# Optimization experiments

Hardware: AMD Instinct MI355X
Metric: run time of the kernel (lower is better)

The kernel has to match this reference:

```python
import jax, jax.numpy as jnp
import numpy as np

N, IN_DIM, OUT_DIM, H = 8192, 512, 512, 1
BN_EPS = 1e-5


def _lin(key, fan_in, fan_out):
    k1, k2 = jax.random.split(key)
    b = 1.0 / np.sqrt(fan_in)
    W = jax.random.uniform(k1, (fan_in, fan_out), jnp.float32, -b, b)
    bias = jax.random.uniform(k2, (fan_out,), jnp.float32, -b, b)
    return W, bias


def setup_inputs() -> dict:
    key = jax.random.key(0)
    ks = jax.random.split(key, 12)
    h = jax.random.normal(ks[0], (N, IN_DIM), jnp.float32)
    A = (jax.random.uniform(ks[1], (N, N)) < 0.01).astype(jnp.float32)
    qw, qb = _lin(ks[2], IN_DIM, OUT_DIM * H)
    kw, kb = _lin(ks[3], IN_DIM, OUT_DIM * H)
    vw, vb = _lin(ks[4], IN_DIM, OUT_DIM * H)
    ow, ob = _lin(ks[5], OUT_DIM, OUT_DIM)
    f1w, f1b = _lin(ks[6], OUT_DIM, OUT_DIM * 2)
    f2w, f2b = _lin(ks[7], OUT_DIM * 2, OUT_DIM)
    bn1_g = jax.random.normal(ks[8], (OUT_DIM,)) * 0.1 + 1.0
    bn1_b = jax.random.normal(ks[9], (OUT_DIM,)) * 0.1
    bn1_m = jax.random.normal(ks[10], (OUT_DIM,)) * 0.1
    bn1_v = jax.random.uniform(ks[11], (OUT_DIM,), jnp.float32, 0.5, 1.5)
    ks2 = jax.random.split(jax.random.fold_in(key, 7), 4)
    bn2_g = jax.random.normal(ks2[0], (OUT_DIM,)) * 0.1 + 1.0
    bn2_b = jax.random.normal(ks2[1], (OUT_DIM,)) * 0.1
    bn2_m = jax.random.normal(ks2[2], (OUT_DIM,)) * 0.1
    bn2_v = jax.random.uniform(ks2[3], (OUT_DIM,), jnp.float32, 0.5, 1.5)
    return dict(A=A, h=h, qw=qw, qb=qb, kw=kw, kb=kb, vw=vw, vb=vb,
                ow=ow, ob=ob, f1w=f1w, f1b=f1b, f2w=f2w, f2b=f2b,
                bn1_g=bn1_g, bn1_b=bn1_b, bn1_m=bn1_m, bn1_v=bn1_v,
                bn2_g=bn2_g, bn2_b=bn2_b, bn2_m=bn2_m, bn2_v=bn2_v)


def _bn_eval(x, g, b, m, v):
    return (x - m) * jax.lax.rsqrt(v + BN_EPS) * g + b


def reference(A, h, qw, qb, kw, kb, vw, vb, ow, ob, f1w, f1b, f2w, f2b,
              bn1_g, bn1_b, bn1_m, bn1_v, bn2_g, bn2_b, bn2_m, bn2_v):
    n = h.shape[0]
    scaling = OUT_DIM ** (-0.5)
    # q/k/v: [N, D, H] as in torch reshape of [N, D*H]
    q = (h @ qw + qb).reshape(n, OUT_DIM, H) * scaling
    k = (h @ kw + kb).reshape(n, OUT_DIM, H)
    v = (h @ vw + vb).reshape(n, OUT_DIM, H)
    qh = jnp.transpose(q, (2, 0, 1))          # (H, N, D)
    kh = jnp.transpose(k, (2, 1, 0))          # (H, D, N)
    vh = jnp.transpose(v, (2, 0, 1))          # (H, N, D)
    attn = jnp.einsum('hnd,hdm->hnm', qh, kh) * A[None]   # (H, N, N)
    attn = jax.nn.softmax(attn, axis=0)        # NOTE: softmax over HEAD axis, as in source
    out = jnp.einsum('hnm,hmd->hnd', attn, vh).reshape(n, H * OUT_DIM)
    # GTLayer (eval mode: dropout = identity, BN uses running stats)
    x = out @ ow + ob
    x = x + h                                  # residual
    x = _bn_eval(x, bn1_g, bn1_b, bn1_m, bn1_v)
    h2 = x
    f = jax.nn.relu(x @ f1w + f1b) @ f2w + f2b
    x = h2 + f
    x = _bn_eval(x, bn2_g, bn2_b, bn2_m, bn2_v)
    return x
```

## Files before the change

kernel.cpp:

```cpp
#include <hip/hip_runtime.h>

#define NROWS 8192
#define DIM 512
#define HID 1024
#define BN_EPS 1e-5f

typedef unsigned short ushort_t;
typedef __attribute__((ext_vector_type(8))) __bf16 bf16x8;
typedef __attribute__((ext_vector_type(4))) float f32x4;

union U4 {
    uint4 u;
    bf16x8 b;
    ushort_t s[8];
};

static __device__ __forceinline__ ushort_t f2b(float f) {
    union { float f; unsigned int i; } c;
    c.f = f;
    unsigned int i = c.i;
    unsigned int r = (i + 0x7FFFu + ((i >> 16) & 1u)) >> 16;
    return (ushort_t)r;
}

static __device__ __forceinline__ void gload_lds16(const ushort_t* g, ushort_t* l) {
    __builtin_amdgcn_global_load_lds((const __attribute__((address_space(1))) void*)g,
                                     (__attribute__((address_space(3))) void*)l, 16, 0, 0);
}

__global__ void colsum_kernel(const float* __restrict__ h, float* __restrict__ hs) {
    __shared__ float red[512];
    int t = threadIdx.x;
    int col0 = (t & 127) * 4;
    int rsub = t >> 7;
    int row0 = blockIdx.x * 32;
    float acc[4] = {0.f, 0.f, 0.f, 0.f};
#pragma unroll
    for (int r = 0; r < 16; ++r) {
        int row = row0 + r * 2 + rsub;
        float4 v = *(const float4*)(h + (size_t)row * DIM + col0);
        acc[0] += v.x; acc[1] += v.y; acc[2] += v.z; acc[3] += v.w;
    }
    if (rsub) {
#pragma unroll
        for (int j = 0; j < 4; ++j) red[col0 + j] = acc[j];
    }
    __syncthreads();
    if (!rsub) {
#pragma unroll
        for (int j = 0; j < 4; ++j) atomicAdd(&hs[col0 + j], acc[j] + red[col0 + j]);
    }
}

__global__ void matvec_kernel(const float* __restrict__ xin, const float* __restrict__ W,
                              const float* __restrict__ bvec, float scaleB,
                              float* __restrict__ outv) {
    __shared__ float red[8][32];
    int t = threadIdx.x;
    int col = blockIdx.x * 32 + (t & 31);
    int ks = t >> 5;
    float s = 0.f;
    for (int ki = 0; ki < 64; ++ki) {
        int k = ks * 64 + ki;
        s += xin[k] * W[k * 512 + col];
    }
    red[ks][t & 31] = s;
    __syncthreads();
    if (ks == 0) {
        float tot = scaleB * bvec[col];
#pragma unroll
        for (int r = 0; r < 8; ++r) tot += red[r][t & 31];
        outv[col] = tot;
    }
}

__global__ void matvec_prep_kernel(const float* __restrict__ xin, const float* __restrict__ W,
                                   const float* __restrict__ bvec,
                                   const float* g1, const float* b1,
                                   const float* m1, const float* v1,
                                   const float* g2, const float* b2,
                                   const float* m2, const float* v2,
                                   float* __restrict__ p, float* __restrict__ q0,
                                   float* __restrict__ a2v, float* __restrict__ c2v) {
    __shared__ float red[8][32];
    int t = threadIdx.x;
    int col = blockIdx.x * 32 + (t & 31);
    int ks = t >> 5;
    float s = 0.f;
    for (int ki = 0; ki < 64; ++ki) {
        int k = ks * 64 + ki;
        s += xin[k] * W[k * 512 + col];
    }
    red[ks][t & 31] = s;
    __syncthreads();
    if (ks == 0) {
        float tot = bvec[col];
#pragma unroll
        for (int r = 0; r < 8; ++r) tot += red[r][t & 31];
        float a1 = g1[col] * rsqrtf(v1[col] + BN_EPS);
        float c1 = b1[col] - m1[col] * a1;
        p[col] = a1;
        q0[col] = tot * a1 + c1;
        float a2 = g2[col] * rsqrtf(v2[col] + BN_EPS);
        a2v[col] = a2;
        c2v[col] = b2[col] - m2[col] * a2;
    }
}

__global__ void misc_kernel(const float* __restrict__ f1w, ushort_t* __restrict__ W1T,
                            const float* __restrict__ f2w, ushort_t* __restrict__ W2T,
                            const float* __restrict__ h, const float* __restrict__ p,
                            const float* __restrict__ q0, ushort_t* __restrict__ x1) {
    __shared__ float tile[32][33];
    int bid = blockIdx.x;
    if (bid >= 1024) {
        int idx = ((bid - 1024) * 256 + threadIdx.x) * 8;
        int d0 = idx & (DIM - 1);
        float4 h0 = *(const float4*)(h + idx);
        float4 h1 = *(const float4*)(h + idx + 4);
        U4 o;
        o.s[0] = f2b(h0.x * p[d0 + 0] + q0[d0 + 0]);
        o.s[1] = f2b(h0.y * p[d0 + 1] + q0[d0 + 1]);
        o.s[2] = f2b(h0.z * p[d0 + 2] + q0[d0 + 2]);
        o.s[3] = f2b(h0.w * p[d0 + 3] + q0[d0 + 3]);
        o.s[4] = f2b(h1.x * p[d0 + 4] + q0[d0 + 4]);
        o.s[5] = f2b(h1.y * p[d0 + 5] + q0[d0 + 5]);
        o.s[6] = f2b(h1.z * p[d0 + 6] + q0[d0 + 6]);
        o.s[7] = f2b(h1.w * p[d0 + 7] + q0[d0 + 7]);
        *(uint4*)(x1 + idx) = o.u;
        return;
    }
    const float* in;
    ushort_t* out;
    int R, C, bx, by;
    if (bid < 512) {
        in = f1w; out = W1T; R = 512; C = 1024;
        bx = (bid & 31) * 32; by = (bid >> 5) * 32;
    } else {
        int b = bid - 512;
        in = f2w; out = W2T; R = 1024; C = 512;
        bx = (b & 15) * 32; by = (b >> 4) * 32;
    }
    int tx = threadIdx.x & 31, ty = threadIdx.x >> 5;
#pragma unroll
    for (int i = 0; i < 32; i += 8)
        tile[ty + i][tx] = in[(by + ty + i) * C + bx + tx];
    __syncthreads();
#pragma unroll
    for (int i = 0; i < 32; i += 8)
        out[(bx + ty + i) * R + by + tx] = f2b(tile[tx][ty + i]);
}

template <int ROWS>
static __device__ __forceinline__ void stage_tile(const ushort_t* __restrict__ g, int ldg,
                                                  ushort_t* lds, int tid) {
#pragma unroll
    for (int it = 0; it < (ROWS * 8) / 256; ++it) {
        int c = it * 256 + tid;
        int row = c >> 3;
        int kc = (c & 7) << 3;
        const ushort_t* gp = g + (size_t)row * ldg + kc;
        ushort_t* lp = lds + ((it * 256 + (tid & 192)) << 3);
        gload_lds16(gp, lp);
    }
}

template <int NJ, bool RELU, bool FUSE>
__global__ __launch_bounds__(256) void gemm_kernel(
    const ushort_t* __restrict__ A, const ushort_t* __restrict__ BT,
    const float* __restrict__ bias, ushort_t* __restrict__ Cb,
    float* __restrict__ Cf, int M, int Nn, int K,
    const float* __restrict__ h, const float* __restrict__ p,
    const float* __restrict__ q0, const float* __restrict__ a2,
    const float* __restrict__ c2) {
    constexpr int BN = NJ * 32;
    constexpr int BK = 64;
    __shared__ ushort_t As[128 * BK];
    __shared__ ushort_t Bs[BN * BK];
    int tid = threadIdx.x;
    int lane = tid & 63, w = tid >> 6;
    int wm = (w & 1) * 64, wn = (w >> 1) * (NJ * 16);
    int bm = blockIdx.y * 128, bn = blockIdx.x * BN;

    f32x4 acc[4][NJ] = {};

    const ushort_t* Ag = A + (size_t)bm * K;
    const ushort_t* Bg = BT + (size_t)bn * K;

    for (int k0 = 0; k0 < K; k0 += BK) {
        __syncthreads();
        stage_tile<128>(Ag + k0, K, As, tid);
        stage_tile<BN>(Bg + k0, K, Bs, tid);
        __syncthreads();
#pragma unroll
        for (int ks = 0; ks < 2; ++ks) {
            int koff = ks * 32 + (lane >> 4) * 8;
            bf16x8 af[4], bfr[NJ];
#pragma unroll
            for (int i = 0; i < 4; ++i) {
                U4 t;
                t.u = *(const uint4*)(As + (wm + i * 16 + (lane & 15)) * BK + koff);
                af[i] = t.b;
            }
#pragma unroll
            for (int j = 0; j < NJ; ++j) {
                U4 t;
                t.u = *(const uint4*)(Bs + (wn + j * 16 + (lane & 15)) * BK + koff);
                bfr[j] = t.b;
            }
#pragma unroll
            for (int i = 0; i < 4; ++i)
#pragma unroll
                for (int j = 0; j < NJ; ++j)
                    acc[i][j] = __builtin_amdgcn_mfma_f32_16x16x32_bf16(af[i], bfr[j], acc[i][j], 0, 0, 0);
        }
    }

#pragma unroll
    for (int i = 0; i < 4; ++i) {
        int row0 = bm + wm + i * 16 + (lane >> 4) * 4;
#pragma unroll
        for (int j = 0; j < NJ; ++j) {
            int col = bn + wn + j * 16 + (lane & 15);
            float bv = bias[col];
            if constexpr (FUSE) {
                float pv = p[col], qv = q0[col], av = a2[col], cv = c2[col];
#pragma unroll
                for (int r = 0; r < 4; ++r) {
                    int row = row0 + r;
                    float hv = h[(size_t)row * DIM + col];
                    float x1v = hv * pv + qv;
                    Cf[(size_t)row * Nn + col] = (x1v + acc[i][j][r] + bv) * av + cv;
                }
            } else {
#pragma unroll
                for (int r = 0; r < 4; ++r) {
                    float v = acc[i][j][r] + bv;
                    if (RELU) v = fmaxf(v, 0.f);
                    Cb[(size_t)(row0 + r) * Nn + col] = f2b(v);
                }
            }
        }
    }
}

extern "C" void kernel_launch(void* const* d_in, const int* in_sizes, int n_in,
                              void* d_out, int out_size, void* d_ws, size_t ws_size,
                              hipStream_t stream) {
    const float* h = (const float*)d_in[1];
    const float* vw = (const float*)d_in[6];
    const float* vb = (const float*)d_in[7];
    const float* ow = (const float*)d_in[8];
    const float* ob = (const float*)d_in[9];
    const float* f1w = (const float*)d_in[10];
    const float* f1b = (const float*)d_in[11];
    const float* f2w = (const float*)d_in[12];
    const float* f2b = (const float*)d_in[13];
    const float* g1 = (const float*)d_in[14];
    const float* b1 = (const float*)d_in[15];
    const float* m1 = (const float*)d_in[16];
    const float* v1 = (const float*)d_in[17];
    const float* g2 = (const float*)d_in[18];
    const float* b2 = (const float*)d_in[19];
    const float* m2 = (const float*)d_in[20];
    const float* v2 = (const float*)d_in[21];
    float* out = (float*)d_out;

    char* ws = (char*)d_ws;
    float* hs = (float*)(ws + 0);
    float* pC = (float*)(ws + 2048);
    float* q0C = (float*)(ws + 4096);
    float* a2C = (float*)(ws + 6144);
    float* c2C = (float*)(ws + 8192);
    float* sBuf = (float*)(ws + 10240);
    ushort_t* X1 = (ushort_t*)(ws + 16384);
    ushort_t* Z = X1 + (size_t)NROWS * DIM;
    ushort_t* W1T = Z + (size_t)NROWS * HID;
    ushort_t* W2T = W1T + (size_t)HID * DIM;

    hipMemsetAsync(hs, 0, 512 * sizeof(float), stream);
    colsum_kernel<<<256, 256, 0, stream>>>(h, hs);
    matvec_kernel<<<16, 256, 0, stream>>>(hs, vw, vb, 8192.0f, sBuf);
    matvec_prep_kernel<<<16, 256, 0, stream>>>(sBuf, ow, ob, g1, b1, m1, v1,
                                               g2, b2, m2, v2, pC, q0C, a2C, c2C);
    misc_kernel<<<3072, 256, 0, stream>>>(f1w, W1T, f2w, W2T, h, pC, q0C, X1);
    gemm_kernel<4, true, false><<<dim3(8, 64), 256, 0, stream>>>(
        X1, W1T, f1b, Z, nullptr, NROWS, HID, DIM,
        nullptr, nullptr, nullptr, nullptr, nullptr);
    gemm_kernel<2, false, true><<<dim3(8, 64), 256, 0, stream>>>(
        Z, W2T, f2b, nullptr, out, NROWS, DIM, HID,
        h, pC, q0C, a2C, c2C);
}
```

Measured before the change: 428.9 us.

## Merge memset, column-sum and two matvec kernels into one cooperative kernel

```diff
diff --git a/kernel.cpp b/kernel.cpp
--- a/kernel.cpp
+++ b/kernel.cpp
@@ -1,4 +1,7 @@
 #include <hip/hip_runtime.h>
+#include <hip/hip_cooperative_groups.h>
+
+namespace cg = cooperative_groups;
 
 #define NROWS 8192
 #define DIM 512
@@ -28,82 +31,92 @@
                                      (__attribute__((address_space(3))) void*)l, 16, 0, 0);
 }
 
-__global__ void colsum_kernel(const float* __restrict__ h, float* __restrict__ hs) {
+__global__ __launch_bounds__(256) void prep_coop_kernel(
+    const float* __restrict__ h, float* __restrict__ hs,
+    const float* __restrict__ vw, const float* __restrict__ vb,
+    const float* __restrict__ ow, const float* __restrict__ ob,
+    const float* g1, const float* b1, const float* m1, const float* v1,
+    const float* g2, const float* b2, const float* m2, const float* v2,
+    float* __restrict__ sBuf,
+    float* __restrict__ p, float* __restrict__ q0,
+    float* __restrict__ a2v, float* __restrict__ c2v) {
+    cg::grid_group grid = cg::this_grid();
     __shared__ float red[512];
+    __shared__ float red2[8][32];
     int t = threadIdx.x;
-    int col0 = (t & 127) * 4;
-    int rsub = t >> 7;
-    int row0 = blockIdx.x * 32;
-    float acc[4] = {0.f, 0.f, 0.f, 0.f};
-#pragma unroll
-    for (int r = 0; r < 16; ++r) {
-        int row = row0 + r * 2 + rsub;
-        float4 v = *(const float4*)(h + (size_t)row * DIM + col0);
-        acc[0] += v.x; acc[1] += v.y; acc[2] += v.z; acc[3] += v.w;
-    }
-    if (rsub) {
-#pragma unroll
-        for (int j = 0; j < 4; ++j) red[col0 + j] = acc[j];
-    }
-    __syncthreads();
-    if (!rsub) {
-#pragma unroll
-        for (int j = 0; j < 4; ++j) atomicAdd(&hs[col0 + j], acc[j] + red[col0 + j]);
-    }
-}
-
-__global__ void matvec_kernel(const float* __restrict__ xin, const float* __restrict__ W,
-                              const float* __restrict__ bvec, float scaleB,
-                              float* __restrict__ outv) {
-    __shared__ float red[8][32];
-    int t = threadIdx.x;
-    int col = blockIdx.x * 32 + (t & 31);
-    int ks = t >> 5;
-    float s = 0.f;
-    for (int ki = 0; ki < 64; ++ki) {
-        int k = ks * 64 + ki;
-        s += xin[k] * W[k * 512 + col];
-    }
-    red[ks][t & 31] = s;
-    __syncthreads();
-    if (ks == 0) {
-        float tot = scaleB * bvec[col];
-#pragma unroll
-        for (int r = 0; r < 8; ++r) tot += red[r][t & 31];
-        outv[col] = tot;
-    }
-}
-
-__global__ void matvec_prep_kernel(const float* __restrict__ xin, const float* __restrict__ W,
-                                   const float* __restrict__ bvec,
-                                   const float* g1, const float* b1,
-                                   const float* m1, const float* v1,
-                                   const float* g2, const float* b2,
-                                   const float* m2, const float* v2,
-                                   float* __restrict__ p, float* __restrict__ q0,
-                                   float* __restrict__ a2v, float* __restrict__ c2v) {
-    __shared__ float red[8][32];
-    int t = threadIdx.x;
-    int col = blockIdx.x * 32 + (t & 31);
-    int ks = t >> 5;
-    float s = 0.f;
-    for (int ki = 0; ki < 64; ++ki) {
-        int k = ks * 64 + ki;
-        s += xin[k] * W[k * 512 + col];
-    }
-    red[ks][t & 31] = s;
-    __syncthreads();
-    if (ks == 0) {
-        float tot = bvec[col];
-#pragma unroll
-        for (int r = 0; r < 8; ++r) tot += red[r][t & 31];
-        float a1 = g1[col] * rsqrtf(v1[col] + BN_EPS);
-        float c1 = b1[col] - m1[col] * a1;
-        p[col] = a1;
-        q0[col] = tot * a1 + c1;
-        float a2 = g2[col] * rsqrtf(v2[col] + BN_EPS);
-        a2v[col] = a2;
-        c2v[col] = b2[col] - m2[col] * a2;
+    int b = blockIdx.x;
+
+    if (b == 0) {
+        hs[t] = 0.f;
+        hs[t + 256] = 0.f;
+    }
+    grid.sync();
+
+    {
+        int col0 = (t & 127) * 4;
+        int rsub = t >> 7;
+        int row0 = b * 32;
+        float acc[4] = {0.f, 0.f, 0.f, 0.f};
+#pragma unroll
+        for (int r = 0; r < 16; ++r) {
+            int row = row0 + r * 2 + rsub;
+            float4 v = *(const float4*)(h + (size_t)row * DIM + col0);
+            acc[0] += v.x; acc[1] += v.y; acc[2] += v.z; acc[3] += v.w;
+        }
+        if (rsub) {
+#pragma unroll
+            for (int j = 0; j < 4; ++j) red[col0 + j] = acc[j];
+        }
+        __syncthreads();
+        if (!rsub) {
+#pragma unroll
+            for (int j = 0; j < 4; ++j) atomicAdd(&hs[col0 + j], acc[j] + red[col0 + j]);
+        }
+    }
+    grid.sync();
+
+    if (b < 16) {
+        int col = b * 32 + (t & 31);
+        int ks = t >> 5;
+        float s = 0.f;
+        for (int ki = 0; ki < 64; ++ki) {
+            int k = ks * 64 + ki;
+            s += hs[k] * vw[k * 512 + col];
+        }
+        red2[ks][t & 31] = s;
+        __syncthreads();
+        if (ks == 0) {
+            float tot = 8192.0f * vb[col];
+#pragma unroll
+            for (int r = 0; r < 8; ++r) tot += red2[r][t & 31];
+            sBuf[col] = tot;
+        }
+        __syncthreads();
+    }
+    grid.sync();
+
+    if (b < 16) {
+        int col = b * 32 + (t & 31);
+        int ks = t >> 5;
+        float s = 0.f;
+        for (int ki = 0; ki < 64; ++ki) {
+            int k = ks * 64 + ki;
+            s += sBuf[k] * ow[k * 512 + col];
+        }
+        red2[ks][t & 31] = s;
+        __syncthreads();
+        if (ks == 0) {
+            float tot = ob[col];
+#pragma unroll
+            for (int r = 0; r < 8; ++r) tot += red2[r][t & 31];
+            float a1 = g1[col] * rsqrtf(v1[col] + BN_EPS);
+            float c1 = b1[col] - m1[col] * a1;
+            p[col] = a1;
+            q0[col] = tot * a1 + c1;
+            float a2 = g2[col] * rsqrtf(v2[col] + BN_EPS);
+            a2v[col] = a2;
+            c2v[col] = b2[col] - m2[col] * a2;
+        }
     }
 }
 
@@ -278,11 +291,13 @@
     ushort_t* W1T = Z + (size_t)NROWS * HID;
     ushort_t* W2T = W1T + (size_t)HID * DIM;
 
-    hipMemsetAsync(hs, 0, 512 * sizeof(float), stream);
-    colsum_kernel<<<256, 256, 0, stream>>>(h, hs);
-    matvec_kernel<<<16, 256, 0, stream>>>(hs, vw, vb, 8192.0f, sBuf);
-    matvec_prep_kernel<<<16, 256, 0, stream>>>(sBuf, ow, ob, g1, b1, m1, v1,
-                                               g2, b2, m2, v2, pC, q0C, a2C, c2C);
+    void* cargs[] = {(void*)&h, (void*)&hs, (void*)&vw, (void*)&vb,
+                     (void*)&ow, (void*)&ob,
+                     (void*)&g1, (void*)&b1, (void*)&m1, (void*)&v1,
+                     (void*)&g2, (void*)&b2, (void*)&m2, (void*)&v2,
+                     (void*)&sBuf, (void*)&pC, (void*)&q0C, (void*)&a2C, (void*)&c2C};
+    hipLaunchCooperativeKernel((void*)prep_coop_kernel, dim3(256), dim3(256),
+                               cargs, 0, stream);
     misc_kernel<<<3072, 256, 0, stream>>>(f1w, W1T, f2w, W2T, h, pC, q0C, X1);
     gemm_kernel<4, true, false><<<dim3(8, 64), 256, 0, stream>>>(
         X1, W1T, f1b, Z, nullptr, NROWS, HID, DIM,
```

Result: slower. 516.2 us (+20.4%).

## Fuse matvec chain with grid barrier and move weight transpose into colsum kernel

Applied to the files above, without the earlier changes.

```diff
diff --git a/kernel.cpp b/kernel.cpp
--- a/kernel.cpp
+++ b/kernel.cpp
@@ -28,127 +28,138 @@
                                      (__attribute__((address_space(3))) void*)l, 16, 0, 0);
 }
 
-__global__ void colsum_kernel(const float* __restrict__ h, float* __restrict__ hs) {
+__global__ void colsum_tr_kernel(const float* __restrict__ h, float* __restrict__ hs,
+                                 const float* __restrict__ f1w, ushort_t* __restrict__ W1T,
+                                 const float* __restrict__ f2w, ushort_t* __restrict__ W2T) {
     __shared__ float red[512];
+    __shared__ float tile[32][33];
+    int bid = blockIdx.x;
     int t = threadIdx.x;
-    int col0 = (t & 127) * 4;
-    int rsub = t >> 7;
-    int row0 = blockIdx.x * 32;
-    float acc[4] = {0.f, 0.f, 0.f, 0.f};
-#pragma unroll
-    for (int r = 0; r < 16; ++r) {
-        int row = row0 + r * 2 + rsub;
-        float4 v = *(const float4*)(h + (size_t)row * DIM + col0);
-        acc[0] += v.x; acc[1] += v.y; acc[2] += v.z; acc[3] += v.w;
-    }
-    if (rsub) {
-#pragma unroll
-        for (int j = 0; j < 4; ++j) red[col0 + j] = acc[j];
-    }
+    if (bid < 256) {
+        int col0 = (t & 127) * 4;
+        int rsub = t >> 7;
+        int row0 = bid * 32;
+        float acc[4] = {0.f, 0.f, 0.f, 0.f};
+#pragma unroll
+        for (int r = 0; r < 16; ++r) {
+            int row = row0 + r * 2 + rsub;
+            float4 v = *(const float4*)(h + (size_t)row * DIM + col0);
+            acc[0] += v.x; acc[1] += v.y; acc[2] += v.z; acc[3] += v.w;
+        }
+        if (rsub) {
+#pragma unroll
+            for (int j = 0; j < 4; ++j) red[col0 + j] = acc[j];
+        }
+        __syncthreads();
+        if (!rsub) {
+#pragma unroll
+            for (int j = 0; j < 4; ++j) atomicAdd(&hs[col0 + j], acc[j] + red[col0 + j]);
+        }
+        return;
+    }
+    const float* in;
+    ushort_t* out;
+    int R, C, bx, by;
+    if (bid < 768) {
+        int b = bid - 256;
+        in = f1w; out = W1T; R = 512; C = 1024;
+        bx = (b & 31) * 32; by = (b >> 5) * 32;
+    } else {
+        int b = bid - 768;
+        in = f2w; out = W2T; R = 1024; C = 512;
+        bx = (b & 15) * 32; by = (b >> 4) * 32;
+    }
+    int tx = t & 31, ty = t >> 5;
+#pragma unroll
+    for (int i = 0; i < 32; i += 8)
+        tile[ty + i][tx] = in[(by + ty + i) * C + bx + tx];
     __syncthreads();
-    if (!rsub) {
-#pragma unroll
-        for (int j = 0; j < 4; ++j) atomicAdd(&hs[col0 + j], acc[j] + red[col0 + j]);
-    }
-}
-
-__global__ void matvec_kernel(const float* __restrict__ xin, const float* __restrict__ W,
-                              const float* __restrict__ bvec, float scaleB,
-                              float* __restrict__ outv) {
+#pragma unroll
+    for (int i = 0; i < 32; i += 8)
+        out[(bx + ty + i) * R + by + tx] = f2b(tile[tx][ty + i]);
+}
+
+__global__ void chain_kernel(const float* __restrict__ hs,
+                             const float* __restrict__ vw, const float* __restrict__ vb,
+                             const float* __restrict__ ow, const float* __restrict__ ob,
+                             const float* g1, const float* b1,
+                             const float* m1, const float* v1,
+                             const float* g2, const float* b2,
+                             const float* m2, const float* v2,
+                             float* __restrict__ sBuf, int* __restrict__ bar,
+                             float* __restrict__ p, float* __restrict__ q0,
+                             float* __restrict__ a2v, float* __restrict__ c2v) {
     __shared__ float red[8][32];
     int t = threadIdx.x;
     int col = blockIdx.x * 32 + (t & 31);
     int ks = t >> 5;
-    float s = 0.f;
-    for (int ki = 0; ki < 64; ++ki) {
-        int k = ks * 64 + ki;
-        s += xin[k] * W[k * 512 + col];
-    }
-    red[ks][t & 31] = s;
+
+    {
+        float s = 0.f;
+        for (int ki = 0; ki < 64; ++ki) {
+            int k = ks * 64 + ki;
+            s += hs[k] * vw[k * 512 + col];
+        }
+        red[ks][t & 31] = s;
+        __syncthreads();
+        if (ks == 0) {
+            float tot = 8192.0f * vb[col];
+#pragma unroll
+            for (int r = 0; r < 8; ++r) tot += red[r][t & 31];
+            __hip_atomic_store(&sBuf[col], tot, __ATOMIC_RELEASE, __HIP_MEMORY_SCOPE_AGENT);
+        }
+        __syncthreads();
+    }
+
+    if (t == 0) {
+        __hip_atomic_fetch_add(bar, 1, __ATOMIC_ACQ_REL, __HIP_MEMORY_SCOPE_AGENT);
+        long spins = 0;
+        while (__hip_atomic_load(bar, __ATOMIC_ACQUIRE, __HIP_MEMORY_SCOPE_AGENT) < 16 &&
+               spins < 200000000L)
+            ++spins;
+    }
     __syncthreads();
-    if (ks == 0) {
-        float tot = scaleB * bvec[col];
-#pragma unroll
-        for (int r = 0; r < 8; ++r) tot += red[r][t & 31];
-        outv[col] = tot;
-    }
-}
-
-__global__ void matvec_prep_kernel(const float* __restrict__ xin, const float* __restrict__ W,
-                                   const float* __restrict__ bvec,
-                                   const float* g1, const float* b1,
-                                   const float* m1, const float* v1,
-                                   const float* g2, const float* b2,
-                                   const float* m2, const float* v2,
-                                   float* __restrict__ p, float* __restrict__ q0,
-                                   float* __restrict__ a2v, float* __restrict__ c2v) {
-    __shared__ float red[8][32];
-    int t = threadIdx.x;
-    int col = blockIdx.x * 32 + (t & 31);
-    int ks = t >> 5;
-    float s = 0.f;
-    for (int ki = 0; ki < 64; ++ki) {
-        int k = ks * 64 + ki;
-        s += xin[k] * W[k * 512 + col];
-    }
-    red[ks][t & 31] = s;
-    __syncthreads();
-    if (ks == 0) {
-        float tot = bvec[col];
-#pragma unroll
-        for (int r = 0; r < 8; ++r) tot += red[r][t & 31];
-        float a1 = g1[col] * rsqrtf(v1[col] + BN_EPS);
-        float c1 = b1[col] - m1[col] * a1;
-        p[col] = a1;
-        q0[col] = tot * a1 + c1;
-        float a2 = g2[col] * rsqrtf(v2[col] + BN_EPS);
-        a2v[col] = a2;
-        c2v[col] = b2[col] - m2[col] * a2;
-    }
-}
-
-__global__ void misc_kernel(const float* __restrict__ f1w, ushort_t* __restrict__ W1T,
-                            const float* __restrict__ f2w, ushort_t* __restrict__ W2T,
-                            const float* __restrict__ h, const float* __restrict__ p,
-                            const float* __restrict__ q0, ushort_t* __restrict__ x1) {
-    __shared__ float tile[32][33];
-    int bid = blockIdx.x;
-    if (bid >= 1024) {
-        int idx = ((bid - 1024) * 256 + threadIdx.x) * 8;
-        int d0 = idx & (DIM - 1);
-        float4 h0 = *(const float4*)(h + idx);
-        float4 h1 = *(const float4*)(h + idx + 4);
-        U4 o;
-        o.s[0] = f2b(h0.x * p[d0 + 0] + q0[d0 + 0]);
-        o.s[1] = f2b(h0.y * p[d0 + 1] + q0[d0 + 1]);
-        o.s[2] = f2b(h0.z * p[d0 + 2] + q0[d0 + 2]);
-        o.s[3] = f2b(h0.w * p[d0 + 3] + q0[d0 + 3]);
-        o.s[4] = f2b(h1.x * p[d0 + 4] + q0[d0 + 4]);
-        o.s[5] = f2b(h1.y * p[d0 + 5] + q0[d0 + 5]);
-        o.s[6] = f2b(h1.z * p[d0 + 6] + q0[d0 + 6]);
-        o.s[7] = f2b(h1.w * p[d0 + 7] + q0[d0 + 7]);
-        *(uint4*)(x1 + idx) = o.u;
-        return;
-    }
-    const float* in;
-    ushort_t* out;
-    int R, C, bx, by;
-    if (bid < 512) {
-        in = f1w; out = W1T; R = 512; C = 1024;
-        bx = (bid & 31) * 32; by = (bid >> 5) * 32;
-    } else {
-        int b = bid - 512;
-        in = f2w; out = W2T; R = 1024; C = 512;
-        bx = (b & 15) * 32; by = (b >> 4) * 32;
-    }
-    int tx = threadIdx.x & 31, ty = threadIdx.x >> 5;
-#pragma unroll
-    for (int i = 0; i < 32; i += 8)
-        tile[ty + i][tx] = in[(by + ty + i) * C + bx + tx];
-    __syncthreads();
-#pragma unroll
-    for (int i = 0; i < 32; i += 8)
-        out[(bx + ty + i) * R + by + tx] = f2b(tile[tx][ty + i]);
+
+    {
+        float s = 0.f;
+        for (int ki = 0; ki < 64; ++ki) {
+            int k = ks * 64 + ki;
+            float sv = __hip_atomic_load(&sBuf[k], __ATOMIC_ACQUIRE, __HIP_MEMORY_SCOPE_AGENT);
+            s += sv * ow[k * 512 + col];
+        }
+        red[ks][t & 31] = s;
+        __syncthreads();
+        if (ks == 0) {
+            float tot = ob[col];
+#pragma unroll
+            for (int r = 0; r < 8; ++r) tot += red[r][t & 31];
+            float a1 = g1[col] * rsqrtf(v1[col] + BN_EPS);
+            float c1 = b1[col] - m1[col] * a1;
+            p[col] = a1;
+            q0[col] = tot * a1 + c1;
+            float a2 = g2[col] * rsqrtf(v2[col] + BN_EPS);
+            a2v[col] = a2;
+            c2v[col] = b2[col] - m2[col] * a2;
+        }
+    }
+}
+
+__global__ void x1_kernel(const float* __restrict__ h, const float* __restrict__ p,
+                          const float* __restrict__ q0, ushort_t* __restrict__ x1) {
+    int idx = (blockIdx.x * blockDim.x + threadIdx.x) * 8;
+    int d0 = idx & (DIM - 1);
+    float4 h0 = *(const float4*)(h + idx);
+    float4 h1 = *(const float4*)(h + idx + 4);
+    U4 o;
+    o.s[0] = f2b(h0.x * p[d0 + 0] + q0[d0 + 0]);
+    o.s[1] = f2b(h0.y * p[d0 + 1] + q0[d0 + 1]);
+    o.s[2] = f2b(h0.z * p[d0 + 2] + q0[d0 + 2]);
+    o.s[3] = f2b(h0.w * p[d0 + 3] + q0[d0 + 3]);
+    o.s[4] = f2b(h1.x * p[d0 + 4] + q0[d0 + 4]);
+    o.s[5] = f2b(h1.y * p[d0 + 5] + q0[d0 + 5]);
+    o.s[6] = f2b(h1.z * p[d0 + 6] + q0[d0 + 6]);
+    o.s[7] = f2b(h1.w * p[d0 + 7] + q0[d0 + 7]);
+    *(uint4*)(x1 + idx) = o.u;
 }
 
 template <int ROWS>
@@ -268,22 +279,23 @@
 
     char* ws = (char*)d_ws;
     float* hs = (float*)(ws + 0);
-    float* pC = (float*)(ws + 2048);
-    float* q0C = (float*)(ws + 4096);
-    float* a2C = (float*)(ws + 6144);
-    float* c2C = (float*)(ws + 8192);
-    float* sBuf = (float*)(ws + 10240);
+    int* bar = (int*)(ws + 2048);
+    float* pC = (float*)(ws + 4096);
+    float* q0C = (float*)(ws + 6144);
+    float* a2C = (float*)(ws + 8192);
+    float* c2C = (float*)(ws + 10240);
+    float* sBuf = (float*)(ws + 12288);
     ushort_t* X1 = (ushort_t*)(ws + 16384);
     ushort_t* Z = X1 + (size_t)NROWS * DIM;
     ushort_t* W1T = Z + (size_t)NROWS * HID;
     ushort_t* W2T = W1T + (size_t)HID * DIM;
 
-    hipMemsetAsync(hs, 0, 512 * sizeof(float), stream);
-    colsum_kernel<<<256, 256, 0, stream>>>(h, hs);
-    matvec_kernel<<<16, 256, 0, stream>>>(hs, vw, vb, 8192.0f, sBuf);
-    matvec_prep_kernel<<<16, 256, 0, stream>>>(sBuf, ow, ob, g1, b1, m1, v1,
-                                               g2, b2, m2, v2, pC, q0C, a2C, c2C);
-    misc_kernel<<<3072, 256, 0, stream>>>(f1w, W1T, f2w, W2T, h, pC, q0C, X1);
+    hipMemsetAsync(ws, 0, 2052, stream);
+    colsum_tr_kernel<<<1280, 256, 0, stream>>>(h, hs, f1w, W1T, f2w, W2T);
+    chain_kernel<<<16, 256, 0, stream>>>(hs, vw, vb, ow, ob,
+                                         g1, b1, m1, v1, g2, b2, m2, v2,
+                                         sBuf, bar, pC, q0C, a2C, c2C);
+    x1_kernel<<<2048, 256, 0, stream>>>(h, pC, q0C, X1);
     gemm_kernel<4, true, false><<<dim3(8, 64), 256, 0, stream>>>(
         X1, W1T, f1b, Z, nullptr, NROWS, HID, DIM,
         nullptr, nullptr, nullptr, nullptr, nullptr);
```

New measurement: 477.8 us. 11.4% more time.
